# Kernel tuning notes

Hardware: AMD Instinct MI355X
Metric: run time of the kernel (lower is better)

The kernel has to match this reference:

```python
import jax, jax.numpy as jnp
import numpy as np

DIM = 1024
NUM_HEADS = 16
HD = DIM // NUM_HEADS  # 64
ROPE_DIM = 64
ROPE_BASE = 10000.0


def setup_inputs() -> dict:
    key = jax.random.key(0)
    ks = jax.random.split(key, 5)
    B, N = 2, 2048
    s = 0.02
    return {
        "x": jax.random.normal(ks[0], (B, N, DIM), dtype=jnp.float32),
        "qkv_w": jax.random.normal(ks[1], (3 * DIM, DIM), dtype=jnp.float32) * s,
        "qkv_b": jax.random.normal(ks[2], (3 * DIM,), dtype=jnp.float32) * s,
        "proj_w": jax.random.normal(ks[3], (DIM, DIM), dtype=jnp.float32) * s,
        "proj_b": jax.random.normal(ks[4], (DIM,), dtype=jnp.float32) * s,
    }


def _apply_rope(t):
    # t: [B, H, N, D] with D even; interleaved (even, odd) pair rotation
    D = t.shape[-1]
    N = t.shape[2]
    pos = jnp.arange(N, dtype=t.dtype)
    inv = 1.0 / (ROPE_BASE ** (jnp.arange(0, D, 2, dtype=t.dtype) / D))
    freqs = pos[:, None] * inv[None, :]          # [N, D/2]
    cos = jnp.cos(freqs)[None, None]             # [1,1,N,D/2]
    sin = jnp.sin(freqs)[None, None]
    e = t[..., 0::2]
    o = t[..., 1::2]
    eo = e * cos - o * sin
    oo = e * sin + o * cos
    return jnp.stack([eo, oo], axis=-1).reshape(t.shape)


def reference(x, qkv_w, qkv_b, proj_w, proj_b):
    B, N, C = x.shape
    H, D = NUM_HEADS, HD
    scale = D ** -0.5
    qkv = x @ qkv_w.T + qkv_b                     # [B,N,3C]
    qkv = qkv.reshape(B, N, 3, H, D).transpose(2, 0, 3, 1, 4)  # [3,B,H,N,D]
    q, k, v = qkv[0], qkv[1], qkv[2]
    # RoPE on first ROPE_DIM dims of each head (here ROPE_DIM == HD)
    q = jnp.concatenate([_apply_rope(q[..., :ROPE_DIM]), q[..., ROPE_DIM:]], axis=-1)
    k = jnp.concatenate([_apply_rope(k[..., :ROPE_DIM]), k[..., ROPE_DIM:]], axis=-1)
    attn = jnp.einsum('bhnd,bhmd->bhnm', q, k) * scale
    attn = jax.nn.softmax(attn, axis=-1)
    out = jnp.einsum('bhnm,bhmd->bhnd', attn, v)  # [B,H,N,D]
    out = out.transpose(0, 2, 1, 3).reshape(B, N, C)
    return out @ proj_w.T + proj_b
```

## Files before the change

### kernel.cpp

```cpp
#include <hip/hip_runtime.h>
#include <hip/hip_bf16.h>
#include <stdint.h>

#define DIM   1024
#define NH    16
#define HDIM  64
#define SEQ   2048
#define BATCH 2
#define BHN   32
#define MTOK  4096
#define SC2   0.18033688f

using u16 = unsigned short;
using u32 = unsigned int;
typedef __attribute__((ext_vector_type(8))) short short8;
typedef __attribute__((ext_vector_type(4))) float f32x4;
typedef __attribute__((ext_vector_type(16))) float f32x16;

__device__ __forceinline__ u16 f2bf(float f) {
  __hip_bfloat16 h = __float2bfloat16(f);
  return *reinterpret_cast<u16*>(&h);
}
__device__ __forceinline__ float bf2f(u16 u) {
  u32 v = ((u32)u) << 16;
  return __builtin_bit_cast(float, v);
}
__device__ __forceinline__ u32 pk2(float lo, float hi) {
  return (u32)f2bf(lo) | ((u32)f2bf(hi) << 16);
}
__device__ __forceinline__ u32 cvtpk(float lo, float hi) {
  u32 r;
  asm("v_cvt_pk_bf16_f32 %0, %1, %2" : "=v"(r) : "v"(lo), "v"(hi));
  return r;
}

__device__ __forceinline__ void gload16(const void* g, void* lds) {
  __builtin_amdgcn_global_load_lds(
      (const __attribute__((address_space(1))) u32*)g,
      (__attribute__((address_space(3))) u32*)lds, 16, 0, 0);
}

#define PREP_A 1048576
#define PREP_B 1835008
#define PREP_C 2097152
#define PREP_E 2162688
__global__ void k_prep(const float4* __restrict__ x, const float4* __restrict__ qw,
                       const float4* __restrict__ pw, ushort4* __restrict__ xb,
                       ushort4* __restrict__ qwb, ushort4* __restrict__ pwb,
                       float2* __restrict__ tab) {
  int i = blockIdx.x * blockDim.x + threadIdx.x;
  if (i < PREP_A) {
    float4 v = x[i];
    xb[i] = make_ushort4(f2bf(v.x), f2bf(v.y), f2bf(v.z), f2bf(v.w));
  } else if (i < PREP_B) {
    int j = i - PREP_A;
    float4 v = qw[j];
    qwb[j] = make_ushort4(f2bf(v.x), f2bf(v.y), f2bf(v.z), f2bf(v.w));
  } else if (i < PREP_C) {
    int j = i - PREP_B;
    float4 v = pw[j];
    pwb[j] = make_ushort4(f2bf(v.x), f2bf(v.y), f2bf(v.z), f2bf(v.w));
  } else if (i < PREP_E) {
    int j = i - PREP_C;
    int n = j >> 5, f = j & 31;
    float inv = powf(10000.f, -(2.f * f) / 64.f);
    float s, c;
    sincosf((float)n * inv, &s, &c);
    tab[j] = make_float2(c, s);
  }
}

template <int EPI>
__global__ __launch_bounds__(256, 2) void k_gemm(
    const u16* __restrict__ A, const u16* __restrict__ Bt,
    const float* __restrict__ bias, int K,
    float* __restrict__ out_f, u16* __restrict__ qb, u16* __restrict__ kb,
    u16* __restrict__ vtb, const float2* __restrict__ tab) {
  __shared__ u16 As[128 * 64];
  __shared__ u16 Bs[128 * 64];
  const int tid = threadIdx.x;
  const int wid = tid >> 6, lane = tid & 63;
  const int lq = lane & 15, g = lane >> 4;
  const int wr = wid >> 1, wc = wid & 1;
  const int brow = blockIdx.y * 128;
  const int bcol = blockIdx.x * 128;
  f32x4 acc[4][4] = {};
  const u16* Ab = A + (size_t)brow * K;
  const u16* Bb = Bt + (size_t)bcol * K;

  for (int k0 = 0; k0 < K; k0 += 64) {
#pragma unroll
    for (int t = 0; t < 4; t++) {
      int rl = wid * 32 + t * 8 + (lane >> 3);
      int cs = (lane & 7) ^ (rl & 7);
      gload16(Ab + (size_t)rl * K + k0 + cs * 8, &As[(wid * 32 + t * 8) * 64]);
      gload16(Bb + (size_t)rl * K + k0 + cs * 8, &Bs[(wid * 32 + t * 8) * 64]);
    }
    __syncthreads();
#pragma unroll
    for (int kc = 0; kc < 2; kc++) {
      short8 af[4], bfr[4];
#pragma unroll
      for (int mt = 0; mt < 4; mt++) {
        int r = wr * 64 + mt * 16 + lq;
        af[mt] = *reinterpret_cast<const short8*>(&As[r * 64 + (((kc * 4 + g) ^ (r & 7)) * 8)]);
      }
#pragma unroll
      for (int nt = 0; nt < 4; nt++) {
        int r = wc * 64 + nt * 16 + lq;
        bfr[nt] = *reinterpret_cast<const short8*>(&Bs[r * 64 + (((kc * 4 + g) ^ (r & 7)) * 8)]);
      }
#pragma unroll
      for (int mt = 0; mt < 4; mt++)
#pragma unroll
        for (int nt = 0; nt < 4; nt++)
          acc[mt][nt] = __builtin_amdgcn_mfma_f32_16x16x32_bf16(af[mt], bfr[nt], acc[mt][nt], 0, 0, 0);
    }
    __syncthreads();
  }

#pragma unroll
  for (int mt = 0; mt < 4; mt++) {
    int row0 = brow + wr * 64 + mt * 16 + g * 4;
#pragma unroll
    for (int nt = 0; nt < 4; nt++) {
      int col = bcol + wc * 64 + nt * 16 + lq;
      float bv = bias[col];
      float v[4];
#pragma unroll
      for (int r = 0; r < 4; r++) v[r] = acc[mt][nt][r] + bv;
      if (EPI == 0) {
#pragma unroll
        for (int r = 0; r < 4; r++) out_f[(size_t)(row0 + r) * DIM + col] = v[r];
      } else {
        int which = col >> 10, hd = col & 1023, hdh = hd >> 6, d = hd & 63;
        int bb = row0 >> 11, n0 = row0 & 2047;
        if (which == 2) {
          uint2 pv = make_uint2(pk2(v[0], v[1]), pk2(v[2], v[3]));
          *reinterpret_cast<uint2*>(&vtb[(((size_t)bb * NH + hdh) * HDIM + d) * SEQ + n0]) = pv;
        } else {
#pragma unroll
          for (int r = 0; r < 4; r++) {
            int n = n0 + r;
            float p = __shfl_xor(v[r], 1);
            float2 cs = tab[n * 32 + (d >> 1)];
            float vv = (d & 1) ? fmaf(p, cs.y, v[r] * cs.x)
                               : fmaf(-p, cs.y, v[r] * cs.x);
            u16 xo = f2bf(vv);
            if (which == 0) qb[(((size_t)bb * NH + hdh) * SEQ + n) * HDIM + d] = xo;
            else            kb[(((size_t)bb * NH + hdh) * SEQ + n) * HDIM + d] = xo;
          }
        }
      }
    }
  }
}

__global__ __launch_bounds__(256, 2) void k_attn(
    const u16* __restrict__ qg, const u16* __restrict__ kg,
    const u16* __restrict__ vg, u16* __restrict__ aout) {
  __shared__ __align__(16) char smem[49152];
  const int tid = threadIdx.x;
  const int wid = tid >> 6, lane = tid & 63;
  const int l31 = lane & 31, h = lane >> 5;

  const int bid = blockIdx.x;
  const int xcd = bid & 7, slot = bid >> 3;
  const int bh = xcd * 4 + (slot >> 4);
  const int qt = slot & 15;
  const int b = bh >> 4, hh = bh & 15;
  const int q0 = qt * 128 + wid * 32;

  const u16* kbase = kg + (size_t)bh * SEQ * HDIM;
  const u16* vbase = vg + (size_t)bh * HDIM * SEQ;

  const u16* qrow = qg + ((size_t)bh * SEQ + q0 + l31) * HDIM;
  short8 qf[4];
#pragma unroll
  for (int c = 0; c < 4; c++)
    qf[c] = *reinterpret_cast<const short8*>(qrow + c * 16 + h * 8);

  int koff[4];
#pragma unroll
  for (int c = 0; c < 4; c++)
    koff[c] = l31 * 128 + (((2 * c + h) ^ (l31 & 7)) << 4);

  f32x16 oA = {}, oB = {};
  float m = -INFINITY, lsum = 0.f;

  auto stage = [&](int buf, int kv0) {
    char* kd = smem + buf * 16384;
#pragma unroll
    for (int t = 0; t < 2; t++) {
      int rl = wid * 16 + t * 8 + (lane >> 3);
      int cs = (lane & 7) ^ (rl & 7);
      gload16(kbase + (size_t)(kv0 + rl) * HDIM + cs * 8, kd + (wid * 16 + t * 8) * 128);
      gload16(vbase + (size_t)rl * SEQ + kv0 + cs * 8, kd + 8192 + (wid * 16 + t * 8) * 128);
    }
  };

  stage(0, 0);
  stage(1, 64);

  const int NT = SEQ / 64;
  int cur = 0, nxt = 2;
  for (int t = 0; t < NT; ++t) {
    if (t < NT - 1) asm volatile("s_waitcnt vmcnt(4)" ::: "memory");
    else            asm volatile("s_waitcnt vmcnt(0)" ::: "memory");
    __builtin_amdgcn_s_barrier();

    const char* kbp = smem + cur * 16384;
    const char* vbp = kbp + 8192;

    f32x16 s0 = {}, s1 = {};
    __builtin_amdgcn_s_setprio(1);
#pragma unroll
    for (int c = 0; c < 4; c++) {
      short8 k0 = *reinterpret_cast<const short8*>(kbp + koff[c]);
      short8 k1 = *reinterpret_cast<const short8*>(kbp + koff[c] + 4096);
      s0 = __builtin_amdgcn_mfma_f32_32x32x16_bf16(k0, qf[c], s0, 0, 0, 0);
      s1 = __builtin_amdgcn_mfma_f32_32x32x16_bf16(k1, qf[c], s1, 0, 0, 0);
    }
    __builtin_amdgcn_s_setprio(0);

    short8 vf0[4], vf1[4];
#pragma unroll
    for (int c = 0; c < 4; c++) {
      vf0[c] = *reinterpret_cast<const short8*>(vbp + koff[c]);
      vf1[c] = *reinterpret_cast<const short8*>(vbp + koff[c] + 4096);
    }

    if (t + 2 < NT) stage(nxt, (t + 2) * 64);

    float tm[8];
#pragma unroll
    for (int r = 0; r < 8; r++)
      tm[r] = fmaxf(fmaxf(s0[r], s1[r]), fmaxf(s0[r + 8], s1[r + 8]));
    float ta = fmaxf(fmaxf(tm[0], tm[1]), tm[2]);
    float tb = fmaxf(fmaxf(tm[3], tm[4]), tm[5]);
    float tc = fmaxf(tm[6], tm[7]);
    float tmax = fmaxf(fmaxf(ta, tb), tc);
    tmax = fmaxf(tmax, __shfl_xor(tmax, 32));

    float alpha = 1.f;
    if (__any(tmax - m > 61.0f)) {
      float mnew = fmaxf(m, tmax);
      alpha = exp2f((m - mnew) * SC2);
      m = mnew;
#pragma unroll
      for (int r = 0; r < 16; r++) { oA[r] *= alpha; oB[r] *= alpha; }
    }
    const float nms = -m * SC2;
#pragma unroll
    for (int r = 0; r < 16; r++) s0[r] = exp2f(fmaf(s0[r], SC2, nms));
#pragma unroll
    for (int r = 0; r < 16; r++) s1[r] = exp2f(fmaf(s1[r], SC2, nms));
    float pa = 0.f, pb = 0.f, pc = 0.f, pd = 0.f;
#pragma unroll
    for (int r = 0; r < 4; r++) {
      pa += s0[r] + s0[r + 4];
      pb += s0[r + 8] + s0[r + 12];
      pc += s1[r] + s1[r + 4];
      pd += s1[r + 8] + s1[r + 12];
    }
    float psum = (pa + pb) + (pc + pd);
    psum += __shfl_xor(psum, 32);
    lsum = lsum * alpha + psum;

    short8 pf[4];
    {
      union { u32 u[4]; short8 v; } pp;
      u32 a0, a1, b0, b1;
      a0 = cvtpk(s0[0], s0[1]);  a1 = cvtpk(s0[2], s0[3]);
      b0 = cvtpk(s0[4], s0[5]);  b1 = cvtpk(s0[6], s0[7]);
      { auto r0 = __builtin_amdgcn_permlane32_swap(a0, b0, false, false);
        auto r1 = __builtin_amdgcn_permlane32_swap(a1, b1, false, false);
        pp.u[0] = r0[0]; pp.u[1] = r1[0]; pp.u[2] = r0[1]; pp.u[3] = r1[1]; pf[0] = pp.v; }
      a0 = cvtpk(s0[8], s0[9]);   a1 = cvtpk(s0[10], s0[11]);
      b0 = cvtpk(s0[12], s0[13]); b1 = cvtpk(s0[14], s0[15]);
      { auto r0 = __builtin_amdgcn_permlane32_swap(a0, b0, false, false);
        auto r1 = __builtin_amdgcn_permlane32_swap(a1, b1, false, false);
        pp.u[0] = r0[0]; pp.u[1] = r1[0]; pp.u[2] = r0[1]; pp.u[3] = r1[1]; pf[1] = pp.v; }
      a0 = cvtpk(s1[0], s1[1]);  a1 = cvtpk(s1[2], s1[3]);
      b0 = cvtpk(s1[4], s1[5]);  b1 = cvtpk(s1[6], s1[7]);
      { auto r0 = __builtin_amdgcn_permlane32_swap(a0, b0, false, false);
        auto r1 = __builtin_amdgcn_permlane32_swap(a1, b1, false, false);
        pp.u[0] = r0[0]; pp.u[1] = r1[0]; pp.u[2] = r0[1]; pp.u[3] = r1[1]; pf[2] = pp.v; }
      a0 = cvtpk(s1[8], s1[9]);   a1 = cvtpk(s1[10], s1[11]);
      b0 = cvtpk(s1[12], s1[13]); b1 = cvtpk(s1[14], s1[15]);
      { auto r0 = __builtin_amdgcn_permlane32_swap(a0, b0, false, false);
        auto r1 = __builtin_amdgcn_permlane32_swap(a1, b1, false, false);
        pp.u[0] = r0[0]; pp.u[1] = r1[0]; pp.u[2] = r0[1]; pp.u[3] = r1[1]; pf[3] = pp.v; }
    }

    __builtin_amdgcn_s_setprio(1);
#pragma unroll
    for (int c = 0; c < 4; c++) {
      oA = __builtin_amdgcn_mfma_f32_32x32x16_bf16(vf0[c], pf[c], oA, 0, 0, 0);
      oB = __builtin_amdgcn_mfma_f32_32x32x16_bf16(vf1[c], pf[c], oB, 0, 0, 0);
    }
    __builtin_amdgcn_s_setprio(0);

    cur = cur == 2 ? 0 : cur + 1;
    nxt = nxt == 2 ? 0 : nxt + 1;
  }

  float invl = 1.0f / lsum;
  int n = q0 + l31;
  u16* op = aout + ((size_t)(b * SEQ + n)) * DIM + hh * HDIM;
#pragma unroll
  for (int g = 0; g < 4; g++) {
    u32 w0 = pk2(oA[4 * g] * invl, oA[4 * g + 1] * invl);
    u32 w1 = pk2(oA[4 * g + 2] * invl, oA[4 * g + 3] * invl);
    *reinterpret_cast<uint2*>(op + 8 * g + 4 * h) = make_uint2(w0, w1);
    u32 x0 = pk2(oB[4 * g] * invl, oB[4 * g + 1] * invl);
    u32 x1 = pk2(oB[4 * g + 2] * invl, oB[4 * g + 3] * invl);
    *reinterpret_cast<uint2*>(op + 32 + 8 * g + 4 * h) = make_uint2(x0, x1);
  }
}

extern "C" void kernel_launch(void* const* d_in, const int* in_sizes, int n_in,
                              void* d_out, int out_size, void* d_ws, size_t ws_size,
                              hipStream_t stream) {
  (void)in_sizes; (void)n_in; (void)out_size; (void)ws_size;
  const float* x      = (const float*)d_in[0];
  const float* qkv_w  = (const float*)d_in[1];
  const float* qkv_b  = (const float*)d_in[2];
  const float* proj_w = (const float*)d_in[3];
  const float* proj_b = (const float*)d_in[4];
  float* out = (float*)d_out;

  char* w = (char*)d_ws;
  u16* xb     = (u16*)w;  w += (size_t)MTOK * DIM * 2;
  u16* wqkvb  = (u16*)w;  w += (size_t)3 * DIM * DIM * 2;
  u16* wprojb = (u16*)w;  w += (size_t)DIM * DIM * 2;
  u16* qb     = (u16*)w;  w += (size_t)BHN * SEQ * HDIM * 2;
  u16* kb     = (u16*)w;  w += (size_t)BHN * SEQ * HDIM * 2;
  u16* vtb    = (u16*)w;  w += (size_t)BHN * SEQ * HDIM * 2;
  u16* aout   = (u16*)w;  w += (size_t)MTOK * DIM * 2;
  float2* tab = (float2*)w;

  k_prep<<<(PREP_E + 255) / 256, 256, 0, stream>>>(
      (const float4*)x, (const float4*)qkv_w, (const float4*)proj_w,
      (ushort4*)xb, (ushort4*)wqkvb, (ushort4*)wprojb, tab);

  k_gemm<1><<<dim3(3 * DIM / 128, MTOK / 128), 256, 0, stream>>>(
      xb, wqkvb, qkv_b, DIM, nullptr, qb, kb, vtb, tab);

  k_attn<<<512, 256, 0, stream>>>(qb, kb, vtb, aout);

  k_gemm<0><<<dim3(DIM / 128, MTOK / 128), 256, 0, stream>>>(
      aout, wprojb, proj_b, DIM, out, nullptr, nullptr, nullptr, nullptr);
}
```

Baseline: 135.2 us.

## Pre-tile K and V in attention fragment order for contiguous LDS staging

The QKV GEMM epilogue now writes K and V^T in a tiled layout: 64-token tiles split into 8-element chunk groups that match the MFMA fragment order. The attention kernel can then stage each tile with fully contiguous 16-byte global loads and read LDS with plain linear offsets, with no XOR swizzle. The goal is better-coalesced global loads and cheaper address math in the attention loop. The trade-off is scattered 2-byte K stores in the epilogue, and possible LDS bank conflicts, since the swizzle is gone and lanes now read with a 16-byte stride.

Measured after the change: 133.7 us. About the same (-1.1%).

```diff
diff --git a/kernel.cpp b/kernel.cpp
--- a/kernel.cpp
+++ b/kernel.cpp
@@ -20,10 +20,6 @@
 __device__ __forceinline__ u16 f2bf(float f) {
   __hip_bfloat16 h = __float2bfloat16(f);
   return *reinterpret_cast<u16*>(&h);
-}
-__device__ __forceinline__ float bf2f(u16 u) {
-  u32 v = ((u32)u) << 16;
-  return __builtin_bit_cast(float, v);
 }
 __device__ __forceinline__ u32 pk2(float lo, float hi) {
   return (u32)f2bf(lo) | ((u32)f2bf(hi) << 16);
@@ -135,9 +131,11 @@
       } else {
         int which = col >> 10, hd = col & 1023, hdh = hd >> 6, d = hd & 63;
         int bb = row0 >> 11, n0 = row0 & 2047;
+        int bh = bb * NH + hdh;
         if (which == 2) {
           uint2 pv = make_uint2(pk2(v[0], v[1]), pk2(v[2], v[3]));
-          *reinterpret_cast<uint2*>(&vtb[(((size_t)bb * NH + hdh) * HDIM + d) * SEQ + n0]) = pv;
+          size_t idx = ((((size_t)bh * 32 + (n0 >> 6)) * 8 + ((n0 >> 3) & 7)) * 64 + d) * 8 + (n0 & 7);
+          *reinterpret_cast<uint2*>(&vtb[idx]) = pv;
         } else {
 #pragma unroll
           for (int r = 0; r < 4; r++) {
@@ -147,8 +145,12 @@
             float vv = (d & 1) ? fmaf(p, cs.y, v[r] * cs.x)
                                : fmaf(-p, cs.y, v[r] * cs.x);
             u16 xo = f2bf(vv);
-            if (which == 0) qb[(((size_t)bb * NH + hdh) * SEQ + n) * HDIM + d] = xo;
-            else            kb[(((size_t)bb * NH + hdh) * SEQ + n) * HDIM + d] = xo;
+            if (which == 0) {
+              qb[((size_t)bh * SEQ + n) * HDIM + d] = xo;
+            } else {
+              size_t idx = ((((size_t)bh * 32 + (n >> 6)) * 8 + (d >> 3)) * 64 + (n & 63)) * 8 + (d & 7);
+              kb[idx] = xo;
+            }
           }
         }
       }
@@ -172,7 +174,7 @@
   const int q0 = qt * 128 + wid * 32;
 
   const u16* kbase = kg + (size_t)bh * SEQ * HDIM;
-  const u16* vbase = vg + (size_t)bh * HDIM * SEQ;
+  const u16* vbase = vg + (size_t)bh * SEQ * HDIM;
 
   const u16* qrow = qg + ((size_t)bh * SEQ + q0 + l31) * HDIM;
   short8 qf[4];
@@ -183,24 +185,25 @@
   int koff[4];
 #pragma unroll
   for (int c = 0; c < 4; c++)
-    koff[c] = l31 * 128 + (((2 * c + h) ^ (l31 & 7)) << 4);
+    koff[c] = (2 * c + h) * 1024 + l31 * 16;
 
   f32x16 oA = {}, oB = {};
   float m = -INFINITY, lsum = 0.f;
 
-  auto stage = [&](int buf, int kv0) {
+  auto stage = [&](int buf, int tidx) {
     char* kd = smem + buf * 16384;
-#pragma unroll
-    for (int t = 0; t < 2; t++) {
-      int rl = wid * 16 + t * 8 + (lane >> 3);
-      int cs = (lane & 7) ^ (rl & 7);
-      gload16(kbase + (size_t)(kv0 + rl) * HDIM + cs * 8, kd + (wid * 16 + t * 8) * 128);
-      gload16(vbase + (size_t)rl * SEQ + kv0 + cs * 8, kd + 8192 + (wid * 16 + t * 8) * 128);
+    const u16* kt = kbase + (size_t)tidx * 4096 + lane * 8;
+    const u16* vt = vbase + (size_t)tidx * 4096 + lane * 8;
+#pragma unroll
+    for (int i = 0; i < 2; i++) {
+      int g = wid + i * 4;
+      gload16(kt + g * 512, kd + g * 1024);
+      gload16(vt + g * 512, kd + 8192 + g * 1024);
     }
   };
 
   stage(0, 0);
-  stage(1, 64);
+  stage(1, 1);
 
   const int NT = SEQ / 64;
   int cur = 0, nxt = 2;
@@ -217,7 +220,7 @@
 #pragma unroll
     for (int c = 0; c < 4; c++) {
       short8 k0 = *reinterpret_cast<const short8*>(kbp + koff[c]);
-      short8 k1 = *reinterpret_cast<const short8*>(kbp + koff[c] + 4096);
+      short8 k1 = *reinterpret_cast<const short8*>(kbp + koff[c] + 512);
       s0 = __builtin_amdgcn_mfma_f32_32x32x16_bf16(k0, qf[c], s0, 0, 0, 0);
       s1 = __builtin_amdgcn_mfma_f32_32x32x16_bf16(k1, qf[c], s1, 0, 0, 0);
     }
@@ -227,10 +230,10 @@
 #pragma unroll
     for (int c = 0; c < 4; c++) {
       vf0[c] = *reinterpret_cast<const short8*>(vbp + koff[c]);
-      vf1[c] = *reinterpret_cast<const short8*>(vbp + koff[c] + 4096);
-    }
-
-    if (t + 2 < NT) stage(nxt, (t + 2) * 64);
+      vf1[c] = *reinterpret_cast<const short8*>(vbp + koff[c] + 512);
+    }
+
+    if (t + 2 < NT) stage(nxt, t + 2);
 
     float tm[8];
 #pragma unroll
```
